# Optimization experiments

Measured on AMD Instinct MI355X. Metric: run time of the kernel, lower is better.

## Reference

```python
import jax, jax.numpy as jnp
import numpy as np

B, N, C, H = 8, 1025, 512, 8
G = 32  # grid size; S = G*G = N-1


def setup_inputs() -> dict:
    key = jax.random.key(0)
    ks = jax.random.split(key, 5)
    return {
        "x": jax.random.normal(ks[0], (B, N, C), dtype=jnp.float32),
        "qkv_w": jax.random.normal(ks[1], (3 * C, C), dtype=jnp.float32) * (C ** -0.5),
        "proj_w": jax.random.normal(ks[2], (C, C), dtype=jnp.float32) * (C ** -0.5),
        "proj_b": jnp.zeros((C,), dtype=jnp.float32),
        "wg_w": jax.random.normal(ks[3], (H, 64), dtype=jnp.float32) * 0.125,
        "wg_b": jnp.zeros((H,), dtype=jnp.float32),
    }


def _geometry_bias(wg_w, wg_b):
    # BoxRelationalEmbedding on a fixed 32x32 grid; batch-independent, so computed once.
    S = G * G
    xs = jnp.arange(G, dtype=jnp.float32)
    px = jnp.repeat(xs, G)   # px_min: row index per flattened cell
    py = jnp.tile(xs, G)     # py_min: col index per flattened cell
    rx0, ry0 = px / G, py / G
    rx1, ry1 = (px + 1.0) / G, (py + 1.0) / G
    cx = 0.5 * (rx0 + rx1)
    cy = 0.5 * (ry0 + ry1)
    w = rx1 - rx0 + 1.0
    h = ry1 - ry0 + 1.0
    dx = jnp.log(jnp.clip(jnp.abs((cx[:, None] - cx[None, :]) / w[:, None]), 1e-3, None))
    dy = jnp.log(jnp.clip(jnp.abs((cy[:, None] - cy[None, :]) / h[:, None]), 1e-3, None))
    dw = jnp.log(w[:, None] / w[None, :])
    dh = jnp.log(h[:, None] / h[None, :])
    pos = jnp.stack([dx, dy, dw, dh], axis=-1)  # [S,S,4]
    dim_mat = 1.0 / jnp.power(1000.0, jnp.arange(8, dtype=jnp.float32) / 8.0)  # dim_g/8 = 8 freqs
    mul = (100.0 * pos)[..., None] * dim_mat        # [S,S,4,8]
    mul = mul.reshape(S, S, 32)
    emb = jnp.concatenate([jnp.sin(mul), jnp.cos(mul)], axis=-1)  # [S,S,64]
    rgw = jax.nn.relu(jnp.einsum('ijd,hd->hij', emb, wg_w) + wg_b[:, None, None])  # [H,S,S]
    rgw = jnp.log(jnp.clip(rgw, 1e-6, None))
    # pad zero column (dim 3 cat of t1) then zero row (dim 2 cat of t2) -> [H, S+1, S+1]
    return jnp.pad(rgw, ((0, 0), (1, 0), (1, 0)))


def reference(x, qkv_w, proj_w, proj_b, wg_w, wg_b):
    b, n, c = x.shape
    hd = c // H
    scale = hd ** -0.5
    bias = _geometry_bias(wg_w, wg_b)  # [H, n, n]
    qkv = (x @ qkv_w.T).reshape(b, n, 3, H, hd)
    q, k, v = qkv[:, :, 0], qkv[:, :, 1], qkv[:, :, 2]  # each [b,n,H,hd]
    attn = jnp.einsum('bihd,bjhd->bhij', q, k) * scale + bias[None]
    attn = jax.nn.softmax(attn, axis=-1)
    out = jnp.einsum('bhij,bjhd->bihd', attn, v).reshape(b, n, c)
    return out @ proj_w.T + proj_b
```

## Files before the change

kernel.cpp:

```cpp
#include <hip/hip_runtime.h>
#include <hip/hip_bf16.h>
#include <hip/hip_fp16.h>
#include <math.h>

#define B_  8
#define N_  1025
#define C_  512
#define H_  8
#define HD_ 64
#define M_  (B_ * N_)
#define VCS 2560
#define VST 36

typedef __attribute__((ext_vector_type(8))) short short8;
typedef __attribute__((ext_vector_type(4))) float f32x4;
typedef __attribute__((ext_vector_type(4))) unsigned short us4;

__device__ inline unsigned short bf16u(float x) {
    __hip_bfloat16 t = __float2bfloat16(x);
    return *(unsigned short*)&t;
}
__device__ inline float fexp2(float x) {
    float r;
    asm("v_exp_f32 %0, %1" : "=v"(r) : "v"(x));
    return r;
}
__device__ inline float h2f(unsigned short u) {
    __half_raw hr; hr.x = u;
    return __half2float(__half(hr));
}
__device__ inline void load_lds16(const void* g, void* l) {
    __builtin_amdgcn_global_load_lds(
        (const __attribute__((address_space(1))) unsigned int*)g,
        (__attribute__((address_space(3))) unsigned int*)l, 16, 0, 0);
}

#define PER_ ((size_t)B_ * H_ * N_ * HD_)
#define SZ_QKVW (3 * C_ * C_)
#define SZ_PRJW (C_ * C_)
#define CAST_BLKS ((4198400 + 786432 + 262144) / 4 / 256)
#define EXP_BLKS 256

__global__ void prep_kernel(const float* __restrict__ x,
                            const float* __restrict__ qkv_w,
                            const float* __restrict__ proj_w,
                            const float* __restrict__ wg_w,
                            const float* __restrict__ wg_b,
                            unsigned short* __restrict__ xb,
                            unsigned short* __restrict__ wqkvb,
                            unsigned short* __restrict__ wprjb,
                            unsigned short* __restrict__ big) {
    __shared__ float tl[1024];
    __shared__ float sT[256], cT[256];
    int blk = blockIdx.x;
    int tid = threadIdx.x;
    if (blk < EXP_BLKS) {
        int h = blk >> 5, rs = blk & 31;
        const float* w = wg_w + h * 64;
        if (tid < 256) {
            const float fr[8] = {1.0f, 0.421696503f, 0.177827941f, 0.074989421f,
                                 0.031622777f, 0.013335214f, 0.005623413f, 0.002371374f};
            int a = tid >> 3, k = tid & 7;
            float dxv = logf(fmaxf((float)a * (1.0f / 33.0f), 0.001f));
            float ang = 100.0f * dxv * fr[k];
            sT[tid] = sinf(ang);
            cT[tid] = cosf(ang);
        }
        __syncthreads();
        float wb = wg_b[h];
        float wtail = 0.f;
#pragma unroll
        for (int k = 0; k < 8; k++) wtail += w[48 + k] + w[56 + k];
#pragma unroll 1
        for (int e = tid; e < 1024; e += 256) {
            int a = e >> 5, b = e & 31;
            float acc = wb + wtail;
#pragma unroll
            for (int k = 0; k < 8; k++) {
                acc += w[k]      * sT[a * 8 + k];
                acc += w[8 + k]  * sT[b * 8 + k];
                acc += w[32 + k] * cT[a * 8 + k];
                acc += w[40 + k] * cT[b * 8 + k];
            }
            tl[e] = log2f(fmaxf(fmaxf(acc, 0.0f), 1e-6f));
        }
        __syncthreads();
        int rbase = rs * 36;
#pragma unroll 1
        for (int e8 = tid; e8 < 36 * 132; e8 += 256) {
            int rr = e8 / 132;
            int cg = e8 - rr * 132;
            int r = rbase + rr;
            int c0 = cg * 8;
            int i = min(r, 1024) - 1;
            int ix = i >> 5, iy = i & 31;
            unsigned short o8[8];
#pragma unroll
            for (int e = 0; e < 8; e++) {
                int c = c0 + e;
                float v;
                if (r == 0 || c == 0) v = 0.f;
                else if (c > 1024)    v = -60000.f;
                else {
                    int j = c - 1;
                    int da = __sad(ix, j >> 5, 0u);
                    int db = __sad(iy, j & 31, 0u);
                    v = tl[da * 32 + db];
                }
                __half hv = __float2half(v);
                o8[e] = *(unsigned short*)&hv;
            }
            *(short8*)(big + ((size_t)h * 1152 + r) * 1056 + c0) = *(short8*)o8;
        }
        return;
    }
    long i4 = ((long)(blk - EXP_BLKS) * 256 + tid) * 4;
    const float* src;
    unsigned short* dst;
    long off;
    if (i4 < (long)PER_)                    { src = x;      dst = xb;    off = i4; }
    else if (i4 < (long)PER_ + SZ_QKVW)     { src = qkv_w;  dst = wqkvb; off = i4 - PER_; }
    else                                    { src = proj_w; dst = wprjb; off = i4 - PER_ - SZ_QKVW; }
    float4 v = *(const float4*)(src + off);
    ushort4 p;
    p.x = bf16u(v.x); p.y = bf16u(v.y); p.z = bf16u(v.z); p.w = bf16u(v.w);
    *(ushort4*)(dst + off) = p;
}

#define GK 512

__global__ __launch_bounds__(256) void gemm_qkv_mfma(
        const unsigned short* __restrict__ A, const unsigned short* __restrict__ W,
        unsigned short* __restrict__ qb, unsigned short* __restrict__ kb,
        unsigned short* __restrict__ vtc) {
    __shared__ __align__(16) unsigned short As[2][128 * 32];
    __shared__ __align__(16) unsigned short Bs[2][128 * 32];
    int tid = threadIdx.x;
    int w = tid >> 6, lane = tid & 63;
    int quad = lane >> 4, l16 = lane & 15;
    int m0 = blockIdx.y * 128;
    int n0 = blockIdx.x * 128;
    int wr = (w >> 1) * 64, wc = (w & 1) * 64;

    int c0 = tid, c1 = tid + 256;
    int a_r0 = min(m0 + (c0 >> 2), M_ - 1), a_c0 = (c0 & 3) * 8;
    int a_r1 = min(m0 + (c1 >> 2), M_ - 1), a_c1 = (c1 & 3) * 8;
    int b_r0 = n0 + (c0 >> 2), b_r1 = n0 + (c1 >> 2);

    int which = n0 >> 9;
    int h = ((n0 + wc) >> 6) & 7;

    f32x4 acc[4][4];
    const f32x4 zero4 = {0.f, 0.f, 0.f, 0.f};
#pragma unroll
    for (int mi = 0; mi < 4; mi++)
#pragma unroll
        for (int ni = 0; ni < 4; ni++) acc[mi][ni] = zero4;

    auto stage = [&](int k0, int buf) {
        load_lds16(A + (size_t)a_r0 * GK + k0 + a_c0, &As[buf][w * 512]);
        load_lds16(A + (size_t)a_r1 * GK + k0 + a_c1, &As[buf][2048 + w * 512]);
        load_lds16(W + (size_t)b_r0 * GK + k0 + a_c0, &Bs[buf][w * 512]);
        load_lds16(W + (size_t)b_r1 * GK + k0 + a_c1, &Bs[buf][2048 + w * 512]);
    };
    stage(0, 0);

    for (int k0 = 0; k0 < GK; k0 += 32) {
        int buf = (k0 >> 5) & 1;
        __syncthreads();
        if (k0 + 32 < GK) stage(k0 + 32, buf ^ 1);
        short8 af[4], bf[4];
#pragma unroll
        for (int mi = 0; mi < 4; mi++)
            af[mi] = *(const short8*)&As[buf][(wr + mi * 16 + l16) * 32 + quad * 8];
#pragma unroll
        for (int ni = 0; ni < 4; ni++)
            bf[ni] = *(const short8*)&Bs[buf][(wc + ni * 16 + l16) * 32 + quad * 8];
#pragma unroll
        for (int mi = 0; mi < 4; mi++)
#pragma unroll
            for (int ni = 0; ni < 4; ni++)
                acc[mi][ni] = __builtin_amdgcn_mfma_f32_16x16x32_bf16(
                    bf[ni], af[mi], acc[mi][ni], 0, 0, 0);
    }

    if (which < 2) {
        unsigned short* dst = (which == 0) ? qb : kb;
        float sc = (which == 0) ? 0.18033688f : 1.0f;
#pragma unroll
        for (int mi = 0; mi < 4; mi++) {
            int m = m0 + wr + mi * 16 + l16;
            if (m < M_) {
                int bb = m / N_;
                int i  = m - bb * N_;
                unsigned short* row = dst + ((size_t)(bb * H_ + h) * N_ + i) * HD_;
#pragma unroll
                for (int ni = 0; ni < 4; ni++) {
                    ushort4 pk;
                    pk.x = bf16u(acc[mi][ni][0] * sc);
                    pk.y = bf16u(acc[mi][ni][1] * sc);
                    pk.z = bf16u(acc[mi][ni][2] * sc);
                    pk.w = bf16u(acc[mi][ni][3] * sc);
                    *(ushort4*)(row + ni * 16 + quad * 4) = pk;
                }
            }
        }
    } else {
#pragma unroll
        for (int mi = 0; mi < 4; mi++) {
            int m = m0 + wr + mi * 16 + l16;
            if (m < M_) {
                int bb = m / N_;
                int i  = m - bb * N_;
                int ch = i >> 5, key = i & 31;
                int slot = ((key >> 2) & 3) * 8 + ((key >> 4) << 2) + (key & 3);
                unsigned short* base = vtc + ((size_t)(bb * H_ + h) * VST + ch) * VCS + slot;
#pragma unroll
                for (int ni = 0; ni < 4; ni++)
#pragma unroll
                    for (int reg = 0; reg < 4; reg++)
                        base[(ni * 16 + quad * 4 + reg) * 40] = bf16u(acc[mi][ni][reg]);
            }
        }
    }
}

__global__ __launch_bounds__(256) void gemm_proj_mfma(
        const unsigned short* __restrict__ A, const unsigned short* __restrict__ W,
        const float* __restrict__ bias, float* __restrict__ out) {
    __shared__ __align__(16) unsigned short As[2][128 * 32];
    __shared__ __align__(16) unsigned short Bs[2][128 * 32];
    int tid = threadIdx.x;
    int w = tid >> 6, lane = tid & 63;
    int quad = lane >> 4, l16 = lane & 15;
    int m0 = blockIdx.y * 128;
    int n0 = blockIdx.x * 128;
    int wr = (w >> 1) * 64, wc = (w & 1) * 64;

    int c0 = tid, c1 = tid + 256;
    int a_r0 = min(m0 + (c0 >> 2), M_ - 1), a_c0 = (c0 & 3) * 8;
    int a_r1 = min(m0 + (c1 >> 2), M_ - 1), a_c1 = (c1 & 3) * 8;
    int b_r0 = n0 + (c0 >> 2), b_r1 = n0 + (c1 >> 2);

    f32x4 acc[4][4];
    const f32x4 zero4 = {0.f, 0.f, 0.f, 0.f};
#pragma unroll
    for (int mi = 0; mi < 4; mi++)
#pragma unroll
        for (int ni = 0; ni < 4; ni++) acc[mi][ni] = zero4;

    auto stage = [&](int k0, int buf) {
        load_lds16(A + (size_t)a_r0 * GK + k0 + a_c0, &As[buf][w * 512]);
        load_lds16(A + (size_t)a_r1 * GK + k0 + a_c1, &As[buf][2048 + w * 512]);
        load_lds16(W + (size_t)b_r0 * GK + k0 + a_c0, &Bs[buf][w * 512]);
        load_lds16(W + (size_t)b_r1 * GK + k0 + a_c1, &Bs[buf][2048 + w * 512]);
    };
    stage(0, 0);

    for (int k0 = 0; k0 < GK; k0 += 32) {
        int buf = (k0 >> 5) & 1;
        __syncthreads();
        if (k0 + 32 < GK) stage(k0 + 32, buf ^ 1);
        short8 af[4], bf[4];
#pragma unroll
        for (int mi = 0; mi < 4; mi++)
            af[mi] = *(const short8*)&As[buf][(wr + mi * 16 + l16) * 32 + quad * 8];
#pragma unroll
        for (int ni = 0; ni < 4; ni++)
            bf[ni] = *(const short8*)&Bs[buf][(wc + ni * 16 + l16) * 32 + quad * 8];
#pragma unroll
        for (int mi = 0; mi < 4; mi++)
#pragma unroll
            for (int ni = 0; ni < 4; ni++)
                acc[mi][ni] = __builtin_amdgcn_mfma_f32_16x16x32_bf16(
                    af[mi], bf[ni], acc[mi][ni], 0, 0, 0);
    }

    float bvals[4];
#pragma unroll
    for (int ni = 0; ni < 4; ni++) bvals[ni] = bias[n0 + wc + ni * 16 + l16];
#pragma unroll
    for (int mi = 0; mi < 4; mi++)
#pragma unroll
        for (int reg = 0; reg < 4; reg++) {
            int m = m0 + wr + mi * 16 + quad * 4 + reg;
            if (m < M_) {
                float* row = out + (size_t)m * C_ + n0 + wc;
#pragma unroll
                for (int ni = 0; ni < 4; ni++)
                    row[ni * 16 + l16] = acc[mi][ni][reg] + bvals[ni];
            }
        }
}

#define RT_ 288

__global__ __launch_bounds__(576, 3) void attn_fused(
        const unsigned short* __restrict__ qg,
        const unsigned short* __restrict__ kg,
        const unsigned short* __restrict__ vtc,
        const unsigned short* __restrict__ bigtab,
        unsigned short* __restrict__ ob) {
    __shared__ __align__(16) unsigned short Ks[2][6144];
    __shared__ __align__(16) unsigned short Vs[2][7680];

    int tid = threadIdx.x;
    int w = tid >> 6, lane = tid & 63;
    int quad = lane >> 4, l16 = lane & 15;

    int lin = blockIdx.x;
    int bh = lin & 63;
    int mt = lin >> 6;
    int b = bh >> 3, h = bh & 7;

    const unsigned short* qp = qg + (size_t)bh * N_ * HD_;
    const unsigned short* kp = kg + (size_t)bh * N_ * HD_;
    const unsigned short* vp = vtc + (size_t)bh * VST * VCS;

    int qrA = mt * RT_ + w * 32 + l16;
    const unsigned short* btA = bigtab + ((size_t)h * 1152 + qrA) * 1056 + quad * 4;
    const unsigned short* btB = btA + (size_t)16 * 1056;

    short8 qfA[2], qfB[2];
    {
        int rowA = min(qrA, N_ - 1);
        int rowB = min(qrA + 16, N_ - 1);
        qfA[0] = *(const short8*)(qp + (size_t)rowA * HD_ + quad * 8);
        qfA[1] = *(const short8*)(qp + (size_t)rowA * HD_ + 32 + quad * 8);
        qfB[0] = *(const short8*)(qp + (size_t)rowB * HD_ + quad * 8);
        qfB[1] = *(const short8*)(qp + (size_t)rowB * HD_ + 32 + quad * 8);
    }

    f32x4 oA[4], oB[4], lA, lB;
    const f32x4 zero4 = {0.f, 0.f, 0.f, 0.f};
#pragma unroll
    for (int g2 = 0; g2 < 4; g2++) { oA[g2] = zero4; oB[g2] = zero4; }
    lA = zero4; lB = zero4;
    short8 ones;
    {
        short one_bf = (short)0x3F80;
#pragma unroll
        for (int j = 0; j < 8; j++) ones[j] = one_bf;
    }

    auto stage = [&](int t, int buf) {
#pragma unroll
        for (int r2 = 0; r2 < 3; r2++) {
            int cb = w * 3 + r2;
            if (cb < 12) {
                int ch = cb * 64 + lane;
                int ct = ch >> 7, rem = ch & 127;
                int oct = rem >> 4, k16 = rem & 15;
                int key = min(t * 96 + ct * 16 + k16, N_ - 1);
                load_lds16(kp + (size_t)key * HD_ + oct * 8, &Ks[buf][cb * 512]);
            } else {
                int vb = cb - 12;
                load_lds16(vp + (size_t)t * 3 * VCS + (size_t)(vb * 64 + lane) * 8,
                           &Vs[buf][vb * 512]);
            }
        }
    };

    us4 bAc[6], bAn[6];
#pragma unroll
    for (int i = 0; i < 6; i++)
        bAn[i] = *(const us4*)(btA + (i >> 1) * 32 + (i & 1) * 16);
    stage(0, 0);

#pragma unroll 1
    for (int t = 0; t < 11; t++) {
        int buf = t & 1;
        __syncthreads();

#pragma unroll
        for (int i = 0; i < 6; i++) bAc[i] = bAn[i];
        us4 bB[6];
        {
            const unsigned short* btp = btB + t * 96;
#pragma unroll
            for (int i = 0; i < 6; i++)
                bB[i] = *(const us4*)(btp + (i >> 1) * 32 + (i & 1) * 16);
        }
        if (t < 10) {
            const unsigned short* btp = btA + (t + 1) * 96;
#pragma unroll
            for (int i = 0; i < 6; i++)
                bAn[i] = *(const us4*)(btp + (i >> 1) * 32 + (i & 1) * 16);
            stage(t + 1, buf ^ 1);
        }

#pragma unroll
        for (int ks = 0; ks < 3; ks++) {
            f32x4 sA[2], sB[2];
#pragma unroll
            for (int ctl = 0; ctl < 2; ctl++) {
                int ct = ks * 2 + ctl;
                short8 kf0 = *(const short8*)&Ks[buf][(ct * 128 + quad * 16 + l16) * 8];
                short8 kf1 = *(const short8*)&Ks[buf][(ct * 128 + (4 + quad) * 16 + l16) * 8];
                sA[ctl] = __builtin_amdgcn_mfma_f32_16x16x32_bf16(kf0, qfA[0], zero4, 0, 0, 0);
                sA[ctl] = __builtin_amdgcn_mfma_f32_16x16x32_bf16(kf1, qfA[1], sA[ctl], 0, 0, 0);
                sB[ctl] = __builtin_amdgcn_mfma_f32_16x16x32_bf16(kf0, qfB[0], zero4, 0, 0, 0);
                sB[ctl] = __builtin_amdgcn_mfma_f32_16x16x32_bf16(kf1, qfB[1], sB[ctl], 0, 0, 0);
            }
            const unsigned short* vcp = &Vs[buf][ks * 2560 + quad * 8];
            short8 vf[4];
#pragma unroll
            for (int g2 = 0; g2 < 4; g2++)
                vf[g2] = *(const short8*)(vcp + (g2 * 16 + l16) * 40);

            short8 pfA;
#pragma unroll
            for (int e = 0; e < 8; e++) {
                int par = e >> 2, r = e & 3;
                float bia = h2f(bAc[ks * 2 + par][r]);
                pfA[e] = (short)bf16u(fexp2(sA[par][r] + bia));
            }
            __builtin_amdgcn_s_setprio(1);
#pragma unroll
            for (int g2 = 0; g2 < 4; g2++)
                oA[g2] = __builtin_amdgcn_mfma_f32_16x16x32_bf16(pfA, vf[g2], oA[g2], 0, 0, 0);
            lA = __builtin_amdgcn_mfma_f32_16x16x32_bf16(pfA, ones, lA, 0, 0, 0);
            __builtin_amdgcn_s_setprio(0);

            short8 pfB;
#pragma unroll
            for (int e = 0; e < 8; e++) {
                int par = e >> 2, r = e & 3;
                float bia = h2f(bB[ks * 2 + par][r]);
                pfB[e] = (short)bf16u(fexp2(sB[par][r] + bia));
            }
            __builtin_amdgcn_s_setprio(1);
#pragma unroll
            for (int g2 = 0; g2 < 4; g2++)
                oB[g2] = __builtin_amdgcn_mfma_f32_16x16x32_bf16(pfB, vf[g2], oB[g2], 0, 0, 0);
            lB = __builtin_amdgcn_mfma_f32_16x16x32_bf16(pfB, ones, lB, 0, 0, 0);
            __builtin_amdgcn_s_setprio(0);
        }
    }

#pragma unroll
    for (int grp = 0; grp < 2; grp++) {
        int rbase = mt * RT_ + w * 32 + grp * 16 + quad * 4;
        const f32x4* oX = grp ? oB : oA;
        const f32x4& lX = grp ? lB : lA;
#pragma unroll
        for (int reg = 0; reg < 4; reg++) {
            int r = rbase + reg;
            if (r < N_) {
                float inv = 1.0f / lX[reg];
                unsigned short* orow = ob + ((size_t)b * N_ + r) * C_ + h * HD_ + l16;
#pragma unroll
                for (int g2 = 0; g2 < 4; g2++)
                    orow[g2 * 16] = bf16u(oX[g2][reg] * inv);
            }
        }
    }
}

extern "C" void kernel_launch(void* const* d_in, const int* in_sizes, int n_in,
                              void* d_out, int out_size, void* d_ws, size_t ws_size,
                              hipStream_t stream) {
    const float* x      = (const float*)d_in[0];
    const float* qkv_w  = (const float*)d_in[1];
    const float* proj_w = (const float*)d_in[2];
    const float* proj_b = (const float*)d_in[3];
    const float* wg_w   = (const float*)d_in[4];
    const float* wg_b   = (const float*)d_in[5];
    float* out = (float*)d_out;

    const size_t per = PER_;
    char* ws = (char*)d_ws;
    unsigned short* bigtab = (unsigned short*)ws;
    unsigned short* xb     = bigtab + (size_t)8 * 1152 * 1056;
    unsigned short* wqkvb  = xb + per;
    unsigned short* wprjb  = wqkvb + (size_t)SZ_QKVW;
    unsigned short* qb     = wprjb + (size_t)SZ_PRJW;
    unsigned short* kb     = qb + per;
    unsigned short* vtc    = kb + per;
    unsigned short* ob     = vtc + (size_t)64 * VST * VCS;

    prep_kernel<<<EXP_BLKS + CAST_BLKS, 256, 0, stream>>>(x, qkv_w, proj_w, wg_w, wg_b,
                                                          xb, wqkvb, wprjb, bigtab);
    gemm_qkv_mfma<<<dim3(12, 65), 256, 0, stream>>>(xb, wqkvb, qb, kb, vtc);
    attn_fused<<<256, 576, 0, stream>>>(qb, kb, vtc, bigtab, ob);
    gemm_proj_mfma<<<dim3(4, 65), 256, 0, stream>>>(ob, wprjb, proj_b, out);
}
```

Measured before the change: 182.2 us.

## Fuse fp32-to-bf16 casts into GEMM loads and merge prep into QKV kernel

The separate prep kernel that cast x and both weight matrices to bf16 is removed. The QKV GEMM now loads fp32 directly into registers, converts to bf16 and writes the result to LDS through a register-staged double buffer. The geometry-bias blocks are folded into the same launch as extra blocks. The projection GEMM converts its fp32 weights the same way. This drops one kernel launch and the full round trip of the casted tensors through memory, at the cost of doubled global read bytes per GEMM tile, more register pressure, and losing the async global-to-LDS loads on those operands.

```diff
diff --git a/kernel.cpp b/kernel.cpp
--- a/kernel.cpp
+++ b/kernel.cpp
@@ -11,6 +11,10 @@
 #define M_  (B_ * N_)
 #define VCS 2560
 #define VST 36
+#define BW_ 1056
+#define PER_ ((size_t)B_ * H_ * N_ * HD_)
+#define EXP_BLKS 256
+#define GK 512
 
 typedef __attribute__((ext_vector_type(8))) short short8;
 typedef __attribute__((ext_vector_type(4))) float f32x4;
@@ -34,30 +38,32 @@
         (const __attribute__((address_space(1))) unsigned int*)g,
         (__attribute__((address_space(3))) unsigned int*)l, 16, 0, 0);
 }
-
-#define PER_ ((size_t)B_ * H_ * N_ * HD_)
-#define SZ_QKVW (3 * C_ * C_)
-#define SZ_PRJW (C_ * C_)
-#define CAST_BLKS ((4198400 + 786432 + 262144) / 4 / 256)
-#define EXP_BLKS 256
-
-__global__ void prep_kernel(const float* __restrict__ x,
-                            const float* __restrict__ qkv_w,
-                            const float* __restrict__ proj_w,
-                            const float* __restrict__ wg_w,
-                            const float* __restrict__ wg_b,
-                            unsigned short* __restrict__ xb,
-                            unsigned short* __restrict__ wqkvb,
-                            unsigned short* __restrict__ wprjb,
-                            unsigned short* __restrict__ big) {
-    __shared__ float tl[1024];
-    __shared__ float sT[256], cT[256];
-    int blk = blockIdx.x;
+__device__ inline short8 pack8(float4 u0, float4 u1) {
+    short8 r;
+    r[0] = (short)bf16u(u0.x); r[1] = (short)bf16u(u0.y);
+    r[2] = (short)bf16u(u0.z); r[3] = (short)bf16u(u0.w);
+    r[4] = (short)bf16u(u1.x); r[5] = (short)bf16u(u1.y);
+    r[6] = (short)bf16u(u1.z); r[7] = (short)bf16u(u1.w);
+    return r;
+}
+
+__global__ __launch_bounds__(256) void gemm_qkv_mfma(
+        const float* __restrict__ x, const float* __restrict__ qkv_w,
+        const float* __restrict__ wg_w, const float* __restrict__ wg_b,
+        unsigned short* __restrict__ qb, unsigned short* __restrict__ kb,
+        unsigned short* __restrict__ vtc, unsigned short* __restrict__ big) {
+    __shared__ __align__(16) unsigned short As[2][4096];
+    __shared__ __align__(16) unsigned short Bs[2][4096];
+    int lin = blockIdx.x;
     int tid = threadIdx.x;
-    if (blk < EXP_BLKS) {
-        int h = blk >> 5, rs = blk & 31;
+
+    if (lin < EXP_BLKS) {
+        float* tl = (float*)&As[0][0];
+        float* sT = (float*)&Bs[0][0];
+        float* cT = sT + 256;
+        int h = lin >> 5, rs = lin & 31;
         const float* w = wg_w + h * 64;
-        if (tid < 256) {
+        {
             const float fr[8] = {1.0f, 0.421696503f, 0.177827941f, 0.074989421f,
                                  0.031622777f, 0.013335214f, 0.005623413f, 0.002371374f};
             int a = tid >> 3, k = tid & 7;
@@ -110,42 +116,22 @@
                 __half hv = __float2half(v);
                 o8[e] = *(unsigned short*)&hv;
             }
-            *(short8*)(big + ((size_t)h * 1152 + r) * 1056 + c0) = *(short8*)o8;
+            *(short8*)(big + ((size_t)h * 1152 + r) * BW_ + c0) = *(short8*)o8;
         }
         return;
     }
-    long i4 = ((long)(blk - EXP_BLKS) * 256 + tid) * 4;
-    const float* src;
-    unsigned short* dst;
-    long off;
-    if (i4 < (long)PER_)                    { src = x;      dst = xb;    off = i4; }
-    else if (i4 < (long)PER_ + SZ_QKVW)     { src = qkv_w;  dst = wqkvb; off = i4 - PER_; }
-    else                                    { src = proj_w; dst = wprjb; off = i4 - PER_ - SZ_QKVW; }
-    float4 v = *(const float4*)(src + off);
-    ushort4 p;
-    p.x = bf16u(v.x); p.y = bf16u(v.y); p.z = bf16u(v.z); p.w = bf16u(v.w);
-    *(ushort4*)(dst + off) = p;
-}
-
-#define GK 512
-
-__global__ __launch_bounds__(256) void gemm_qkv_mfma(
-        const unsigned short* __restrict__ A, const unsigned short* __restrict__ W,
-        unsigned short* __restrict__ qb, unsigned short* __restrict__ kb,
-        unsigned short* __restrict__ vtc) {
-    __shared__ __align__(16) unsigned short As[2][128 * 32];
-    __shared__ __align__(16) unsigned short Bs[2][128 * 32];
-    int tid = threadIdx.x;
-    int w = tid >> 6, lane = tid & 63;
+
+    int bidx = lin - EXP_BLKS;
+    int bx = bidx % 12, by = bidx / 12;
+    int wv = tid >> 6, lane = tid & 63;
     int quad = lane >> 4, l16 = lane & 15;
-    int m0 = blockIdx.y * 128;
-    int n0 = blockIdx.x * 128;
-    int wr = (w >> 1) * 64, wc = (w & 1) * 64;
-
-    int c0 = tid, c1 = tid + 256;
-    int a_r0 = min(m0 + (c0 >> 2), M_ - 1), a_c0 = (c0 & 3) * 8;
-    int a_r1 = min(m0 + (c1 >> 2), M_ - 1), a_c1 = (c1 & 3) * 8;
-    int b_r0 = n0 + (c0 >> 2), b_r1 = n0 + (c1 >> 2);
+    int m0 = by * 128, n0 = bx * 128;
+    int wr = (wv >> 1) * 64, wc = (wv & 1) * 64;
+
+    int ar0 = min(m0 + (tid >> 2), M_ - 1);
+    int ar1 = min(m0 + 64 + (tid >> 2), M_ - 1);
+    int br0 = n0 + (tid >> 2), br1 = n0 + 64 + (tid >> 2);
+    int ac = (tid & 3) * 8;
 
     int which = n0 >> 9;
     int h = ((n0 + wc) >> 6) & 7;
@@ -157,18 +143,30 @@
 #pragma unroll
         for (int ni = 0; ni < 4; ni++) acc[mi][ni] = zero4;
 
-    auto stage = [&](int k0, int buf) {
-        load_lds16(A + (size_t)a_r0 * GK + k0 + a_c0, &As[buf][w * 512]);
-        load_lds16(A + (size_t)a_r1 * GK + k0 + a_c1, &As[buf][2048 + w * 512]);
-        load_lds16(W + (size_t)b_r0 * GK + k0 + a_c0, &Bs[buf][w * 512]);
-        load_lds16(W + (size_t)b_r1 * GK + k0 + a_c1, &Bs[buf][2048 + w * 512]);
-    };
-    stage(0, 0);
+    float4 ra0, ra1, ra2, ra3, rb0, rb1, rb2, rb3;
+    auto loadAll = [&](int k0) {
+        const float* pa0 = x + (size_t)ar0 * GK + k0 + ac;
+        const float* pa1 = x + (size_t)ar1 * GK + k0 + ac;
+        const float* pb0 = qkv_w + (size_t)br0 * GK + k0 + ac;
+        const float* pb1 = qkv_w + (size_t)br1 * GK + k0 + ac;
+        ra0 = *(const float4*)pa0; ra1 = *(const float4*)(pa0 + 4);
+        ra2 = *(const float4*)pa1; ra3 = *(const float4*)(pa1 + 4);
+        rb0 = *(const float4*)pb0; rb1 = *(const float4*)(pb0 + 4);
+        rb2 = *(const float4*)pb1; rb3 = *(const float4*)(pb1 + 4);
+    };
+    auto writeAll = [&](int buf) {
+        *(short8*)&As[buf][tid * 8]        = pack8(ra0, ra1);
+        *(short8*)&As[buf][2048 + tid * 8] = pack8(ra2, ra3);
+        *(short8*)&Bs[buf][tid * 8]        = pack8(rb0, rb1);
+        *(short8*)&Bs[buf][2048 + tid * 8] = pack8(rb2, rb3);
+    };
+    loadAll(0);
+    writeAll(0);
 
     for (int k0 = 0; k0 < GK; k0 += 32) {
         int buf = (k0 >> 5) & 1;
+        if (k0 + 32 < GK) loadAll(k0 + 32);
         __syncthreads();
-        if (k0 + 32 < GK) stage(k0 + 32, buf ^ 1);
         short8 af[4], bf[4];
 #pragma unroll
         for (int mi = 0; mi < 4; mi++)
@@ -182,6 +180,7 @@
             for (int ni = 0; ni < 4; ni++)
                 acc[mi][ni] = __builtin_amdgcn_mfma_f32_16x16x32_bf16(
                     bf[ni], af[mi], acc[mi][ni], 0, 0, 0);
+        if (k0 + 32 < GK) writeAll(buf ^ 1);
     }
 
     if (which < 2) {
@@ -226,10 +225,10 @@
 }
 
 __global__ __launch_bounds__(256) void gemm_proj_mfma(
-        const unsigned short* __restrict__ A, const unsigned short* __restrict__ W,
+        const unsigned short* __restrict__ A, const float* __restrict__ Wf,
         const float* __restrict__ bias, float* __restrict__ out) {
-    __shared__ __align__(16) unsigned short As[2][128 * 32];
-    __shared__ __align__(16) unsigned short Bs[2][128 * 32];
+    __shared__ __align__(16) unsigned short As[2][4096];
+    __shared__ __align__(16) unsigned short Bs[2][4096];
     int tid = threadIdx.x;
     int w = tid >> 6, lane = tid & 63;
     int quad = lane >> 4, l16 = lane & 15;
@@ -237,10 +236,10 @@
     int n0 = blockIdx.x * 128;
     int wr = (w >> 1) * 64, wc = (w & 1) * 64;
 
-    int c0 = tid, c1 = tid + 256;
-    int a_r0 = min(m0 + (c0 >> 2), M_ - 1), a_c0 = (c0 & 3) * 8;
-    int a_r1 = min(m0 + (c1 >> 2), M_ - 1), a_c1 = (c1 & 3) * 8;
-    int b_r0 = n0 + (c0 >> 2), b_r1 = n0 + (c1 >> 2);
+    int ar0 = min(m0 + (tid >> 2), M_ - 1);
+    int ar1 = min(m0 + 64 + (tid >> 2), M_ - 1);
+    int br0 = n0 + (tid >> 2), br1 = n0 + 64 + (tid >> 2);
+    int ac = (tid & 3) * 8;
 
     f32x4 acc[4][4];
     const f32x4 zero4 = {0.f, 0.f, 0.f, 0.f};
@@ -249,18 +248,29 @@
 #pragma unroll
         for (int ni = 0; ni < 4; ni++) acc[mi][ni] = zero4;
 
-    auto stage = [&](int k0, int buf) {
-        load_lds16(A + (size_t)a_r0 * GK + k0 + a_c0, &As[buf][w * 512]);
-        load_lds16(A + (size_t)a_r1 * GK + k0 + a_c1, &As[buf][2048 + w * 512]);
-        load_lds16(W + (size_t)b_r0 * GK + k0 + a_c0, &Bs[buf][w * 512]);
-        load_lds16(W + (size_t)b_r1 * GK + k0 + a_c1, &Bs[buf][2048 + w * 512]);
-    };
-    stage(0, 0);
+    auto stageA = [&](int k0, int buf) {
+        load_lds16(A + (size_t)ar0 * GK + k0 + ac, &As[buf][w * 512]);
+        load_lds16(A + (size_t)ar1 * GK + k0 + ac, &As[buf][2048 + w * 512]);
+    };
+    float4 rw0, rw1, rw2, rw3;
+    auto loadW = [&](int k0) {
+        const float* p0 = Wf + (size_t)br0 * GK + k0 + ac;
+        const float* p1 = Wf + (size_t)br1 * GK + k0 + ac;
+        rw0 = *(const float4*)p0; rw1 = *(const float4*)(p0 + 4);
+        rw2 = *(const float4*)p1; rw3 = *(const float4*)(p1 + 4);
+    };
+    auto writeW = [&](int buf) {
+        *(short8*)&Bs[buf][tid * 8]        = pack8(rw0, rw1);
+        *(short8*)&Bs[buf][2048 + tid * 8] = pack8(rw2, rw3);
+    };
+    stageA(0, 0);
+    loadW(0);
+    writeW(0);
 
     for (int k0 = 0; k0 < GK; k0 += 32) {
         int buf = (k0 >> 5) & 1;
         __syncthreads();
-        if (k0 + 32 < GK) stage(k0 + 32, buf ^ 1);
+        if (k0 + 32 < GK) { stageA(k0 + 32, buf ^ 1); loadW(k0 + 32); }
         short8 af[4], bf[4];
 #pragma unroll
         for (int mi = 0; mi < 4; mi++)
@@ -274,6 +284,7 @@
             for (int ni = 0; ni < 4; ni++)
                 acc[mi][ni] = __builtin_amdgcn_mfma_f32_16x16x32_bf16(
                     af[mi], bf[ni], acc[mi][ni], 0, 0, 0);
+        if (k0 + 32 < GK) writeW(buf ^ 1);
     }
 
     float bvals[4];
@@ -318,8 +329,8 @@
     const unsigned short* vp = vtc + (size_t)bh * VST * VCS;
 
     int qrA = mt * RT_ + w * 32 + l16;
-    const unsigned short* btA = bigtab + ((size_t)h * 1152 + qrA) * 1056 + quad * 4;
-    const unsigned short* btB = btA + (size_t)16 * 1056;
+    const unsigned short* btA = bigtab + ((size_t)h * 1152 + qrA) * BW_ + quad * 4;
+    const unsigned short* btB = btA + (size_t)16 * BW_;
 
     short8 qfA[2], qfB[2];
     {
@@ -471,17 +482,13 @@
     const size_t per = PER_;
     char* ws = (char*)d_ws;
     unsigned short* bigtab = (unsigned short*)ws;
-    unsigned short* xb     = bigtab + (size_t)8 * 1152 * 1056;
-    unsigned short* wqkvb  = xb + per;
-    unsigned short* wprjb  = wqkvb + (size_t)SZ_QKVW;
-    unsigned short* qb     = wprjb + (size_t)SZ_PRJW;
+    unsigned short* qb     = bigtab + (size_t)8 * 1152 * BW_;
     unsigned short* kb     = qb + per;
     unsigned short* vtc    = kb + per;
     unsigned short* ob     = vtc + (size_t)64 * VST * VCS;
 
-    prep_kernel<<<EXP_BLKS + CAST_BLKS, 256, 0, stream>>>(x, qkv_w, proj_w, wg_w, wg_b,
-                                                          xb, wqkvb, wprjb, bigtab);
-    gemm_qkv_mfma<<<dim3(12, 65), 256, 0, stream>>>(xb, wqkvb, qb, kb, vtc);
+    gemm_qkv_mfma<<<EXP_BLKS + 12 * 65, 256, 0, stream>>>(
+        x, qkv_w, wg_w, wg_b, qb, kb, vtc, bigtab);
     attn_fused<<<256, 576, 0, stream>>>(qb, kb, vtc, bigtab, ob);
-    gemm_proj_mfma<<<dim3(4, 65), 256, 0, stream>>>(ob, wprjb, proj_b, out);
-}
+    gemm_proj_mfma<<<dim3(4, 65), 256, 0, stream>>>(ob, proj_w, proj_b, out);
+}
```

After: 184.0 us. Within noise of the previous version (+1.0%).
